# Optimization experiments

Measured on AMD Instinct MI355X. Metric: run time of the kernel, lower is better.

The kernel has to match this reference:

```python
import jax, jax.numpy as jnp
import numpy as np

EPS = 1e-5  # pyg LayerNorm default eps


def _graph_ln(x):
    # pyg.nn.norm.LayerNorm(affine=False), default mode='graph', batch=None:
    # normalizes over ALL elements of the tensor (x - x.mean()) / x.std(unbiased=False)
    m = x.mean()
    v = jnp.mean((x - m) ** 2)
    return (x - m) * jax.lax.rsqrt(v + EPS)


def _cheb_conv(x, row, col, w, W, b):
    # ChebConv, normalization='sym', lambda_max=2 => scaled Laplacian
    # L_hat = L - I = -D^{-1/2} A D^{-1/2} (self-loops removed, weighted)
    # x: [B,N,C_in], row/col: [E], w: [E], W: [K,C_in,C_out], b: [C_out]
    N = x.shape[1]
    w = jnp.where(row == col, 0.0, w)  # remove_self_loops
    deg = jnp.zeros((N,), x.dtype).at[row].add(w)
    dinv = jnp.where(deg > 0, jax.lax.rsqrt(jnp.maximum(deg, 1e-12)), 0.0)
    norm = -(dinv[row] * w * dinv[col])  # [E]

    def prop(t):  # out[i] += norm_e * t[j] for edge (j=row -> i=col)
        msg = norm[None, :, None] * t[:, row, :]  # [B,E,C]
        return jnp.zeros_like(t).at[:, col, :].add(msg)

    Tx0 = x
    out = jnp.einsum('bnc,cd->bnd', Tx0, W[0])
    Tx1 = prop(x)
    out = out + jnp.einsum('bnc,cd->bnd', Tx1, W[1])
    for k in range(2, W.shape[0]):
        Tx2 = 2.0 * prop(Tx1) - Tx0
        out = out + jnp.einsum('bnc,cd->bnd', Tx2, W[k])
        Tx0, Tx1 = Tx1, Tx2
    return out + b


def setup_inputs() -> dict:
    key = jax.random.key(0)
    ks = jax.random.split(key, 8)
    B, N, C, E, L, K = 8, 2048, 256, 32768, 3, 3
    node_feature = jax.random.normal(ks[0], (B, N, C), dtype=jnp.float32)
    edge_index = jax.random.randint(ks[1], (L, 2, E), 0, N)
    edge_weight = jax.random.uniform(ks[2], (L, E), dtype=jnp.float32)
    s = 1.0 / np.sqrt(C)
    cheb_w = jax.random.normal(ks[3], (L, K, C, C), dtype=jnp.float32) * s
    cheb_b = jnp.zeros((L, C), dtype=jnp.float32)
    mlp_w = jax.random.normal(ks[4], (L, C, C), dtype=jnp.float32) * s
    mlp_b = jax.random.normal(ks[5], (L, C), dtype=jnp.float32) * 0.01
    return {"node_feature": node_feature, "edge_weight": edge_weight,
            "cheb_w": cheb_w, "cheb_b": cheb_b, "mlp_w": mlp_w,
            "mlp_b": mlp_b, "edge_index": edge_index}


def reference(node_feature, edge_weight, cheb_w, cheb_b, mlp_w, mlp_b, edge_index):
    h = node_feature  # [B,N,C]
    L = cheb_w.shape[0]
    for l in range(L):
        h_res = h
        hn = _graph_ln(h)
        hc = _cheb_conv(hn, edge_index[l, 0], edge_index[l, 1],
                        edge_weight[l], cheb_w[l], cheb_b[l])
        h = hc + h_res
        h_res = h
        hn = _graph_ln(h)
        hm = jax.nn.gelu(jnp.einsum('bnc,cd->bnd', hn, mlp_w[l]) + mlp_b[l],
                         approximate=False)  # dropout is identity at inference
        h = hm + h_res
    return h.mean(axis=1)  # [B,C]
```

## Files before the change

### kernel.cpp

```cpp
#include <hip/hip_runtime.h>

#define BATCH   8
#define NNODE   2048
#define CH      256
#define NEDGE   32768
#define NLAYER  3
#define MROWS   (NNODE*BATCH)
#define KCAT    (3*CH)
#define NTOT    (MROWS*CH)

typedef _Float16 half8 __attribute__((ext_vector_type(8)));
typedef _Float16 half4 __attribute__((ext_vector_type(4)));
typedef float    f32x4 __attribute__((ext_vector_type(4)));

#define OFF_H      ((size_t)0)
#define OFF_ACAT   ((size_t)16777216)
#define OFF_HF     ((size_t)41943040)
#define OFF_WT     ((size_t)50331648)
#define OFF_MT     ((size_t)51511296)
#define OFF_PARTA  ((size_t)51904512)
#define OFF_PARTB  ((size_t)51912704)
#define OFF_CS     ((size_t)51920896)
#define OFF_CSM    ((size_t)51930112)
#define OFF_DEG    ((size_t)51933184)
#define OFF_CNT    ((size_t)51957760)
#define OFF_ELIST  ((size_t)51982336)
#define OFF_NORM   ((size_t)53555200)
#define OFF_R1     ((size_t)53948416)
#define OFF_R2     ((size_t)53972992)
#define OFF_MP     ((size_t)53997568)

__device__ __forceinline__ void async_lds16(const void* g, void* l) {
  __builtin_amdgcn_global_load_lds((const __attribute__((address_space(1))) void*)g,
                                   (__attribute__((address_space(3))) void*)l, 16, 0, 0);
}

__global__ __launch_bounds__(256) void k_init(const float* __restrict__ x,
                                              float* __restrict__ h,
                                              _Float16* __restrict__ Acat,
                                              float2* __restrict__ part,
                                              float* __restrict__ deg,
                                              unsigned int* __restrict__ count,
                                              float* __restrict__ r1) {
  const int blk = blockIdx.x;
  if (blk < 1024) {
    int tid = blk*256 + threadIdx.x;
    float s = 0.f, s2 = 0.f;
    for (int i = tid; i < NTOT/4; i += 1024*256) {
      int c4 = i & 63, b = (i >> 6) & 7, n = i >> 9;
      float4 v = ((const float4*)x)[((b*NNODE + n) << 6) + c4];
      ((float4*)h)[i] = v;
      half4 o; o[0]=(_Float16)v.x; o[1]=(_Float16)v.y; o[2]=(_Float16)v.z; o[3]=(_Float16)v.w;
      *(half4*)&Acat[(size_t)(i >> 6)*KCAT + c4*4] = o;
      s  += v.x + v.y + v.z + v.w;
      s2 += v.x*v.x + v.y*v.y + v.z*v.z + v.w*v.w;
    }
    __shared__ float rs[512];
    rs[threadIdx.x] = s; rs[256+threadIdx.x] = s2; __syncthreads();
    for (int o = 128; o > 0; o >>= 1) {
      if (threadIdx.x < o) { rs[threadIdx.x] += rs[threadIdx.x+o]; rs[256+threadIdx.x] += rs[256+threadIdx.x+o]; }
      __syncthreads();
    }
    if (threadIdx.x == 0) part[blk] = make_float2(rs[0], rs[256]);
  } else {
    int i = (blk - 1024)*256 + threadIdx.x;
    if (i < NLAYER*NNODE) { deg[i] = 0.f; count[i] = 0u; r1[i] = 0.f; }
  }
}

__global__ __launch_bounds__(256) void k_weights(const float* __restrict__ cheb_w,
                                                 const float* __restrict__ mlp_w,
                                                 _Float16* __restrict__ Wt,
                                                 _Float16* __restrict__ Mt) {
  __shared__ _Float16 lt[64][72];
  const int t = threadIdx.x;
  const int rr = t >> 4, c4 = t & 15;
  const int tile = blockIdx.x;
  if (tile < 144) {
    const int l = tile / 48, rem = tile % 48;
    const int kk = rem / 16, q = rem % 16, ci = q >> 2, ni = q & 3;
    const float4* W  = (const float4*)cheb_w + ((size_t)((l*3 + kk)*CH + ci*64))*64 + ni*16;
    const float4* W2 = (const float4*)cheb_w + ((size_t)((l*3 + 2 )*CH + ci*64))*64 + ni*16;
    #pragma unroll
    for (int p = 0; p < 4; ++p) {
      const int r = p*16 + rr;
      float4 v = W[(size_t)r*64 + c4];
      if (kk == 0) {
        float4 v2 = W2[(size_t)r*64 + c4];
        v.x -= v2.x; v.y -= v2.y; v.z -= v2.z; v.w -= v2.w;
      } else if (kk == 2) {
        v.x *= 2.f; v.y *= 2.f; v.z *= 2.f; v.w *= 2.f;
      }
      lt[c4*4+0][r] = (_Float16)v.x; lt[c4*4+1][r] = (_Float16)v.y;
      lt[c4*4+2][r] = (_Float16)v.z; lt[c4*4+3][r] = (_Float16)v.w;
    }
    __syncthreads();
    const int nr = t >> 2, ch2 = t & 3;
    #pragma unroll
    for (int pp = 0; pp < 2; ++pp) {
      const int ch = ch2 + pp*4;
      half8 v = *(const half8*)&lt[nr][ch*8];
      *(half8*)&Wt[((size_t)(l*CH + ni*64 + nr))*KCAT + kk*256 + ci*64 + ch*8] = v;
    }
  } else {
    const int m = tile - 144;
    const int l = m / 16, q = m % 16, ci = q >> 2, ni = q & 3;
    const float4* W = (const float4*)mlp_w + ((size_t)(l*CH + ci*64))*64 + ni*16;
    #pragma unroll
    for (int p = 0; p < 4; ++p) {
      const int r = p*16 + rr;
      float4 v = W[(size_t)r*64 + c4];
      lt[c4*4+0][r] = (_Float16)v.x; lt[c4*4+1][r] = (_Float16)v.y;
      lt[c4*4+2][r] = (_Float16)v.z; lt[c4*4+3][r] = (_Float16)v.w;
    }
    __syncthreads();
    const int nr = t >> 2, ch2 = t & 3;
    #pragma unroll
    for (int pp = 0; pp < 2; ++pp) {
      const int ch = ch2 + pp*4;
      half8 v = *(const half8*)&lt[nr][ch*8];
      *(half8*)&Mt[((size_t)(l*CH + ni*64 + nr))*CH + ci*64 + ch*8] = v;
    }
  }
}

__global__ __launch_bounds__(256) void k_edge_scatter(const int* __restrict__ ei,
                                                      const float* __restrict__ ew,
                                                      float* deg, unsigned int* count,
                                                      unsigned int* elist) {
  int i = blockIdx.x*256 + threadIdx.x;
  if (i >= NLAYER*NEDGE) return;
  int l = i / NEDGE, e = i % NEDGE;
  const int* rows = ei + l*2*NEDGE;
  const int* cols = rows + NEDGE;
  int r = rows[e], c = cols[e];
  float w = (r == c) ? 0.f : ew[l*NEDGE + e];
  atomicAdd(&deg[l*NNODE + r], w);
  unsigned int slot = atomicAdd(&count[l*NNODE + c], 1u);
  if (slot < 64u) elist[(l*NNODE + c)*64 + slot] = (unsigned int)e;
}

__global__ __launch_bounds__(256) void k_edge_norm(const int* __restrict__ ei,
                                                   const float* __restrict__ ew,
                                                   const float* __restrict__ deg,
                                                   float* __restrict__ norm,
                                                   float* __restrict__ r1) {
  int i = blockIdx.x*256 + threadIdx.x;
  if (i >= NLAYER*NEDGE) return;
  int l = i / NEDGE, e = i % NEDGE;
  const int* rows = ei + l*2*NEDGE;
  const int* cols = rows + NEDGE;
  int r = rows[e], c = cols[e];
  float w = (r == c) ? 0.f : ew[l*NEDGE + e];
  float dr = deg[l*NNODE + r], dc = deg[l*NNODE + c];
  float ir = dr > 0.f ? rsqrtf(fmaxf(dr, 1e-12f)) : 0.f;
  float ic = dc > 0.f ? rsqrtf(fmaxf(dc, 1e-12f)) : 0.f;
  float nm = -(ir * w * ic);
  norm[i] = nm;
  atomicAdd(&r1[l*NNODE + c], nm);
}

__global__ __launch_bounds__(256) void k_aux(const int* __restrict__ ei,
                                             const float* __restrict__ norm,
                                             const unsigned int* __restrict__ count,
                                             const unsigned int* __restrict__ elist,
                                             const float* __restrict__ r1,
                                             float* __restrict__ r2,
                                             const _Float16* __restrict__ Wt,
                                             const _Float16* __restrict__ Mt,
                                             float* __restrict__ cs,
                                             float* __restrict__ csM) {
  const int blk = blockIdx.x;
  if (blk < 24) {
    int i = blk*256 + threadIdx.x;
    int l = i / NNODE;
    const int* rows = ei + l*2*NEDGE;
    unsigned int c = count[i]; if (c > 64u) c = 64u;
    const unsigned int* el = elist + (size_t)i*64;
    float s = 0.f;
    for (unsigned int j = 0; j < c; ++j) {
      unsigned int e = el[j];
      s += norm[l*NEDGE + e] * r1[l*NNODE + rows[e]];
    }
    r2[i] = s;
  } else if (blk < 33) {
    int idx = blk - 24;
    int l = idx / 3, kk = idx % 3, n = threadIdx.x;
    const half8* row = (const half8*)&Wt[((size_t)(l*CH + n))*KCAT + kk*256];
    float s = 0.f;
    #pragma unroll 4
    for (int j = 0; j < 32; ++j) {
      half8 v = row[j];
      s += (float)v[0]+(float)v[1]+(float)v[2]+(float)v[3]
         + (float)v[4]+(float)v[5]+(float)v[6]+(float)v[7];
    }
    cs[(l*3 + kk)*CH + n] = s;
  } else {
    int l = blk - 33, n = threadIdx.x;
    const half8* row = (const half8*)&Mt[((size_t)(l*CH + n))*CH];
    float s = 0.f;
    #pragma unroll 4
    for (int j = 0; j < 32; ++j) {
      half8 v = row[j];
      s += (float)v[0]+(float)v[1]+(float)v[2]+(float)v[3]
         + (float)v[4]+(float)v[5]+(float)v[6]+(float)v[7];
    }
    csM[l*CH + n] = s;
  }
}

template<int SRC_OFF, int DST_OFF>
__global__ __launch_bounds__(64) void k_prop(_Float16* __restrict__ Acat,
                                             const int* __restrict__ rows,
                                             const float* __restrict__ norm,
                                             const unsigned int* __restrict__ count,
                                             const unsigned int* __restrict__ elist) {
  const int blk = blockIdx.x;
  const int b = blk & 7, dst = blk >> 3;
  const int lane = threadIdx.x;
  unsigned int cnt = count[dst]; if (cnt > 64u) cnt = 64u;
  int   srcv = 0;
  float nmv  = 0.f;
  if (lane < (int)cnt) {
    unsigned int e = elist[dst*64 + lane];
    srcv = rows[e];
    nmv  = norm[e];
  }
  float a0 = 0.f, a1 = 0.f, a2 = 0.f, a3 = 0.f;
  const _Float16* base = Acat + SRC_OFF + lane*4;
  #define PROP_STEP(i)                                                              \
    {                                                                               \
      int   src = __builtin_amdgcn_readlane(srcv, (i));                             \
      int   nbi = __builtin_amdgcn_readlane(__builtin_bit_cast(int, nmv), (i));     \
      float nm  = __builtin_bit_cast(float, nbi);                                   \
      half4 v = *(const half4*)&base[(size_t)(src*8 + b)*KCAT];                     \
      a0 += nm*(float)v[0]; a1 += nm*(float)v[1];                                   \
      a2 += nm*(float)v[2]; a3 += nm*(float)v[3];                                   \
    }
  unsigned int i = 0;
  for (; i + 4 <= cnt; i += 4) { PROP_STEP(i) PROP_STEP(i+1) PROP_STEP(i+2) PROP_STEP(i+3) }
  for (; i < cnt; ++i) { PROP_STEP(i) }
  #undef PROP_STEP
  half4 o; o[0] = (_Float16)a0; o[1] = (_Float16)a1; o[2] = (_Float16)a2; o[3] = (_Float16)a3;
  *(half4*)&Acat[(size_t)(dst*8 + b)*KCAT + DST_OFF + lane*4] = o;
}

template<int KSTEPS, int DO_GELU>
__global__ __launch_bounds__(256) void k_gemm(const _Float16* __restrict__ A, int lda,
                                              const _Float16* __restrict__ Bt, int ldb,
                                              const float* __restrict__ bias,
                                              const float* __restrict__ cs,
                                              const float* __restrict__ r1,
                                              const float* __restrict__ r2,
                                              const float2* __restrict__ part_in,
                                              float2* __restrict__ part_out,
                                              float* __restrict__ H,
                                              _Float16* __restrict__ Of, int ofs) {
  __shared__ _Float16 Als[64*64];
  __shared__ _Float16 Bls[64*64];
  __shared__ float red[512];
  __shared__ float mv[2];
  const int bm = blockIdx.x, bn = blockIdx.y;
  const int t = threadIdx.x;
  const int w = t >> 6, lane = t & 63;
  const int quad = lane >> 4, l16 = lane & 15;
  const int wm = w & 1, wn = w >> 1;

  {
    float s = 0.f, s2 = 0.f;
    for (int i = t; i < 1024; i += 256) { float2 p = part_in[i]; s += p.x; s2 += p.y; }
    red[t] = s; red[256+t] = s2; __syncthreads();
    for (int o = 128; o > 0; o >>= 1) {
      if (t < o) { red[t] += red[t+o]; red[256+t] += red[256+t+o]; }
      __syncthreads();
    }
    if (t == 0) {
      float mean = red[0] * (1.f/(float)NTOT);
      float var  = red[256] * (1.f/(float)NTOT) - mean*mean;
      mv[0] = mean; mv[1] = rsqrtf(var + 1e-5f);
    }
    __syncthreads();
  }
  const float mean = mv[0], istd = mv[1];

  f32x4 acc00 = {0.f,0.f,0.f,0.f};
  f32x4 acc01 = acc00, acc10 = acc00, acc11 = acc00;

  const int c0 = w*64 + lane, c1 = 256 + w*64 + lane;
  const int r0 = c0 >> 3, s0 = (c0 & 7) ^ (r0 & 7);
  const int r1i = c1 >> 3, s1 = (c1 & 7) ^ (r1i & 7);
  const _Float16* ga0 = A  + (size_t)(bm*64 + r0)*lda + s0*8;
  const _Float16* ga1 = A  + (size_t)(bm*64 + r1i)*lda + s1*8;
  const _Float16* gb0 = Bt + (size_t)(bn*64 + r0)*ldb + s0*8;
  const _Float16* gb1 = Bt + (size_t)(bn*64 + r1i)*ldb + s1*8;
  _Float16* lA0 = &Als[w*512];
  _Float16* lA1 = &Als[2048 + w*512];
  _Float16* lB0 = &Bls[w*512];
  _Float16* lB1 = &Bls[2048 + w*512];

  const int ra0 = wm*32 + l16, ra1 = ra0 + 16;
  const int rb0 = wn*32 + l16, rb1 = rb0 + 16;

  for (int ks = 0; ks < KSTEPS; ++ks) {
    async_lds16(ga0, lA0); async_lds16(ga1, lA1);
    async_lds16(gb0, lB0); async_lds16(gb1, lB1);
    ga0 += 64; ga1 += 64; gb0 += 64; gb1 += 64;
    __syncthreads();
    #pragma unroll
    for (int kh = 0; kh < 2; ++kh) {
      const int q = kh*4 + quad;
      half8 a0 = *(const half8*)&Als[ra0*64 + (q ^ (ra0 & 7))*8];
      half8 a1 = *(const half8*)&Als[ra1*64 + (q ^ (ra1 & 7))*8];
      half8 b0 = *(const half8*)&Bls[rb0*64 + (q ^ (rb0 & 7))*8];
      half8 b1 = *(const half8*)&Bls[rb1*64 + (q ^ (rb1 & 7))*8];
      acc00 = __builtin_amdgcn_mfma_f32_16x16x32_f16(a0, b0, acc00, 0, 0, 0);
      acc01 = __builtin_amdgcn_mfma_f32_16x16x32_f16(a0, b1, acc01, 0, 0, 0);
      acc10 = __builtin_amdgcn_mfma_f32_16x16x32_f16(a1, b0, acc10, 0, 0, 0);
      acc11 = __builtin_amdgcn_mfma_f32_16x16x32_f16(a1, b1, acc11, 0, 0, 0);
    }
    __syncthreads();
  }

  float s = 0.f, s2 = 0.f;
  const int gm0 = bm*64 + wm*32, gn0 = bn*64 + wn*32;
  const float mi = -mean * istd;
  #pragma unroll
  for (int i = 0; i < 2; ++i) {
    #pragma unroll
    for (int j = 0; j < 2; ++j) {
      f32x4 a = (i == 0) ? (j == 0 ? acc00 : acc01) : (j == 0 ? acc10 : acc11);
      const int col = gn0 + j*16 + l16;
      const float bv = bias[col];
      const float c0v = cs[col];
      float c1v = 0.f, c2v = 0.f;
      if (!DO_GELU) { c1v = cs[256 + col]; c2v = cs[512 + col]; }
      #pragma unroll
      for (int r = 0; r < 4; ++r) {
        const int row = gm0 + i*16 + quad*4 + r;
        float v;
        if (DO_GELU) {
          v = istd*a[r] + mi*c0v + bv;
          v = 0.5f*v*(1.f + erff(v*0.70710678118654752f));
        } else {
          const int node = row >> 3;
          v = istd*a[r] + mi*(c0v + r1[node]*c1v + r2[node]*c2v) + bv;
        }
        float hv = H[(size_t)row*CH + col] + v;
        H[(size_t)row*CH + col] = hv;
        Of[(size_t)row*ofs + col] = (_Float16)hv;
        s += hv; s2 += hv*hv;
      }
    }
  }
  red[t] = s; red[256+t] = s2; __syncthreads();
  for (int o = 128; o > 0; o >>= 1) {
    if (t < o) { red[t] += red[t+o]; red[256+t] += red[256+t+o]; }
    __syncthreads();
  }
  if (t == 0) part_out[blockIdx.y*gridDim.x + blockIdx.x] = make_float2(red[0], red[256]);
}

__global__ __launch_bounds__(256) void k_mean_part(const float* __restrict__ h,
                                                   float* __restrict__ mp) {
  int blk = blockIdx.x;
  int b = blk & 7, chunk = blk >> 3;
  int c = threadIdx.x;
  float s = 0.f;
  for (int k = 0; k < 32; ++k) {
    int n = chunk*32 + k;
    s += h[((size_t)(n*8 + b) << 8) + c];
  }
  mp[((b*64 + chunk) << 8) + c] = s;
}

__global__ __launch_bounds__(256) void k_mean_final(const float* __restrict__ mp,
                                                    float* __restrict__ out) {
  int b = blockIdx.x, c = threadIdx.x;
  float s = 0.f;
  for (int ch = 0; ch < 64; ++ch) s += mp[((b*64 + ch) << 8) + c];
  out[(b << 8) + c] = s * (1.f/(float)NNODE);
}

extern "C" void kernel_launch(void* const* d_in, const int* in_sizes, int n_in,
                              void* d_out, int out_size, void* d_ws, size_t ws_size,
                              hipStream_t stream) {
  const float* x      = (const float*)d_in[0];
  const float* ew     = (const float*)d_in[1];
  const float* cheb_w = (const float*)d_in[2];
  const float* cheb_b = (const float*)d_in[3];
  const float* mlp_w  = (const float*)d_in[4];
  const float* mlp_b  = (const float*)d_in[5];
  const int*   ei     = (const int*)d_in[6];
  float* out = (float*)d_out;

  char* ws = (char*)d_ws;
  float*        h     = (float*)(ws + OFF_H);
  _Float16*     Acat  = (_Float16*)(ws + OFF_ACAT);
  _Float16*     Hf    = (_Float16*)(ws + OFF_HF);
  _Float16*     Wt    = (_Float16*)(ws + OFF_WT);
  _Float16*     Mt    = (_Float16*)(ws + OFF_MT);
  float2*       partA = (float2*)(ws + OFF_PARTA);
  float2*       partB = (float2*)(ws + OFF_PARTB);
  float*        cs    = (float*)(ws + OFF_CS);
  float*        csM   = (float*)(ws + OFF_CSM);
  float*        deg   = (float*)(ws + OFF_DEG);
  unsigned int* cnt   = (unsigned int*)(ws + OFF_CNT);
  unsigned int* elist = (unsigned int*)(ws + OFF_ELIST);
  float*        norm  = (float*)(ws + OFF_NORM);
  float*        r1    = (float*)(ws + OFF_R1);
  float*        r2    = (float*)(ws + OFF_R2);
  float*        mp    = (float*)(ws + OFF_MP);

  k_init<<<1048, 256, 0, stream>>>(x, h, Acat, partA, deg, cnt, r1);
  k_weights<<<192, 256, 0, stream>>>(cheb_w, mlp_w, Wt, Mt);
  k_edge_scatter<<<(NLAYER*NEDGE)/256, 256, 0, stream>>>(ei, ew, deg, cnt, elist);
  k_edge_norm<<<(NLAYER*NEDGE)/256, 256, 0, stream>>>(ei, ew, deg, norm, r1);
  k_aux<<<36, 256, 0, stream>>>(ei, norm, cnt, elist, r1, r2, Wt, Mt, cs, csM);

  for (int l = 0; l < NLAYER; ++l) {
    const int* rows_l = ei + l*2*NEDGE;
    const unsigned int* cnt_l = cnt + l*NNODE;
    const unsigned int* el_l  = elist + (size_t)l*NNODE*64;
    const float* norm_l = norm + l*NEDGE;

    k_prop<0, 256><<<MROWS, 64, 0, stream>>>(Acat, rows_l, norm_l, cnt_l, el_l);
    k_prop<256, 512><<<MROWS, 64, 0, stream>>>(Acat, rows_l, norm_l, cnt_l, el_l);
    k_gemm<12, 0><<<dim3(256, 4), 256, 0, stream>>>(
        Acat, KCAT, Wt + (size_t)l*CH*KCAT, KCAT, cheb_b + l*CH,
        cs + l*3*CH, r1 + l*NNODE, r2 + l*NNODE, partA, partB, h, Hf, CH);
    k_gemm<4, 1><<<dim3(256, 4), 256, 0, stream>>>(
        Hf, CH, Mt + (size_t)l*CH*CH, CH, mlp_b + l*CH,
        csM + l*CH, r1, r2, partB, partA, h, Acat, KCAT);
  }

  k_mean_part<<<512, 256, 0, stream>>>(h, mp);
  k_mean_final<<<8, 256, 0, stream>>>(mp, out);
}
```

Baseline: 317.3 us.

## Fuse all stages into one persistent cooperative kernel with grid syncs

```diff
diff --git a/kernel.cpp b/kernel.cpp
--- a/kernel.cpp
+++ b/kernel.cpp
@@ -1,4 +1,7 @@
 #include <hip/hip_runtime.h>
+#include <hip/hip_cooperative_groups.h>
+
+namespace cg = cooperative_groups;
 
 #define BATCH   8
 #define NNODE   2048
@@ -30,52 +33,21 @@
 #define OFF_R2     ((size_t)53972992)
 #define OFF_MP     ((size_t)53997568)
 
+#define SMEM_BYTES 18448
+
 __device__ __forceinline__ void async_lds16(const void* g, void* l) {
   __builtin_amdgcn_global_load_lds((const __attribute__((address_space(1))) void*)g,
                                    (__attribute__((address_space(3))) void*)l, 16, 0, 0);
 }
 
-__global__ __launch_bounds__(256) void k_init(const float* __restrict__ x,
-                                              float* __restrict__ h,
-                                              _Float16* __restrict__ Acat,
-                                              float2* __restrict__ part,
-                                              float* __restrict__ deg,
-                                              unsigned int* __restrict__ count,
-                                              float* __restrict__ r1) {
-  const int blk = blockIdx.x;
-  if (blk < 1024) {
-    int tid = blk*256 + threadIdx.x;
-    float s = 0.f, s2 = 0.f;
-    for (int i = tid; i < NTOT/4; i += 1024*256) {
-      int c4 = i & 63, b = (i >> 6) & 7, n = i >> 9;
-      float4 v = ((const float4*)x)[((b*NNODE + n) << 6) + c4];
-      ((float4*)h)[i] = v;
-      half4 o; o[0]=(_Float16)v.x; o[1]=(_Float16)v.y; o[2]=(_Float16)v.z; o[3]=(_Float16)v.w;
-      *(half4*)&Acat[(size_t)(i >> 6)*KCAT + c4*4] = o;
-      s  += v.x + v.y + v.z + v.w;
-      s2 += v.x*v.x + v.y*v.y + v.z*v.z + v.w*v.w;
-    }
-    __shared__ float rs[512];
-    rs[threadIdx.x] = s; rs[256+threadIdx.x] = s2; __syncthreads();
-    for (int o = 128; o > 0; o >>= 1) {
-      if (threadIdx.x < o) { rs[threadIdx.x] += rs[threadIdx.x+o]; rs[256+threadIdx.x] += rs[256+threadIdx.x+o]; }
-      __syncthreads();
-    }
-    if (threadIdx.x == 0) part[blk] = make_float2(rs[0], rs[256]);
-  } else {
-    int i = (blk - 1024)*256 + threadIdx.x;
-    if (i < NLAYER*NNODE) { deg[i] = 0.f; count[i] = 0u; r1[i] = 0.f; }
-  }
-}
-
-__global__ __launch_bounds__(256) void k_weights(const float* __restrict__ cheb_w,
-                                                 const float* __restrict__ mlp_w,
-                                                 _Float16* __restrict__ Wt,
-                                                 _Float16* __restrict__ Mt) {
-  __shared__ _Float16 lt[64][72];
-  const int t = threadIdx.x;
+__device__ __forceinline__ void weights_tile(int tile, int t,
+                                             const float* __restrict__ cheb_w,
+                                             const float* __restrict__ mlp_w,
+                                             _Float16* __restrict__ Wt,
+                                             _Float16* __restrict__ Mt,
+                                             char* smem) {
+  _Float16 (*lt)[72] = (_Float16(*)[72])smem;
   const int rr = t >> 4, c4 = t & 15;
-  const int tile = blockIdx.x;
   if (tile < 144) {
     const int l = tile / 48, rem = tile % 48;
     const int kk = rem / 16, q = rem % 16, ci = q >> 2, ni = q & 3;
@@ -124,143 +96,62 @@
   }
 }
 
-__global__ __launch_bounds__(256) void k_edge_scatter(const int* __restrict__ ei,
-                                                      const float* __restrict__ ew,
-                                                      float* deg, unsigned int* count,
-                                                      unsigned int* elist) {
-  int i = blockIdx.x*256 + threadIdx.x;
-  if (i >= NLAYER*NEDGE) return;
-  int l = i / NEDGE, e = i % NEDGE;
-  const int* rows = ei + l*2*NEDGE;
-  const int* cols = rows + NEDGE;
-  int r = rows[e], c = cols[e];
-  float w = (r == c) ? 0.f : ew[l*NEDGE + e];
-  atomicAdd(&deg[l*NNODE + r], w);
-  unsigned int slot = atomicAdd(&count[l*NNODE + c], 1u);
-  if (slot < 64u) elist[(l*NNODE + c)*64 + slot] = (unsigned int)e;
-}
-
-__global__ __launch_bounds__(256) void k_edge_norm(const int* __restrict__ ei,
-                                                   const float* __restrict__ ew,
-                                                   const float* __restrict__ deg,
-                                                   float* __restrict__ norm,
-                                                   float* __restrict__ r1) {
-  int i = blockIdx.x*256 + threadIdx.x;
-  if (i >= NLAYER*NEDGE) return;
-  int l = i / NEDGE, e = i % NEDGE;
-  const int* rows = ei + l*2*NEDGE;
-  const int* cols = rows + NEDGE;
-  int r = rows[e], c = cols[e];
-  float w = (r == c) ? 0.f : ew[l*NEDGE + e];
-  float dr = deg[l*NNODE + r], dc = deg[l*NNODE + c];
-  float ir = dr > 0.f ? rsqrtf(fmaxf(dr, 1e-12f)) : 0.f;
-  float ic = dc > 0.f ? rsqrtf(fmaxf(dc, 1e-12f)) : 0.f;
-  float nm = -(ir * w * ic);
-  norm[i] = nm;
-  atomicAdd(&r1[l*NNODE + c], nm);
-}
-
-__global__ __launch_bounds__(256) void k_aux(const int* __restrict__ ei,
-                                             const float* __restrict__ norm,
-                                             const unsigned int* __restrict__ count,
-                                             const unsigned int* __restrict__ elist,
-                                             const float* __restrict__ r1,
-                                             float* __restrict__ r2,
-                                             const _Float16* __restrict__ Wt,
-                                             const _Float16* __restrict__ Mt,
-                                             float* __restrict__ cs,
-                                             float* __restrict__ csM) {
-  const int blk = blockIdx.x;
-  if (blk < 24) {
-    int i = blk*256 + threadIdx.x;
-    int l = i / NNODE;
-    const int* rows = ei + l*2*NEDGE;
-    unsigned int c = count[i]; if (c > 64u) c = 64u;
-    const unsigned int* el = elist + (size_t)i*64;
-    float s = 0.f;
-    for (unsigned int j = 0; j < c; ++j) {
-      unsigned int e = el[j];
-      s += norm[l*NEDGE + e] * r1[l*NNODE + rows[e]];
-    }
-    r2[i] = s;
-  } else if (blk < 33) {
-    int idx = blk - 24;
-    int l = idx / 3, kk = idx % 3, n = threadIdx.x;
-    const half8* row = (const half8*)&Wt[((size_t)(l*CH + n))*KCAT + kk*256];
-    float s = 0.f;
-    #pragma unroll 4
-    for (int j = 0; j < 32; ++j) {
-      half8 v = row[j];
-      s += (float)v[0]+(float)v[1]+(float)v[2]+(float)v[3]
-         + (float)v[4]+(float)v[5]+(float)v[6]+(float)v[7];
-    }
-    cs[(l*3 + kk)*CH + n] = s;
-  } else {
-    int l = blk - 33, n = threadIdx.x;
-    const half8* row = (const half8*)&Mt[((size_t)(l*CH + n))*CH];
-    float s = 0.f;
-    #pragma unroll 4
-    for (int j = 0; j < 32; ++j) {
-      half8 v = row[j];
-      s += (float)v[0]+(float)v[1]+(float)v[2]+(float)v[3]
-         + (float)v[4]+(float)v[5]+(float)v[6]+(float)v[7];
-    }
-    csM[l*CH + n] = s;
-  }
-}
-
-template<int SRC_OFF, int DST_OFF>
-__global__ __launch_bounds__(64) void k_prop(_Float16* __restrict__ Acat,
-                                             const int* __restrict__ rows,
-                                             const float* __restrict__ norm,
-                                             const unsigned int* __restrict__ count,
-                                             const unsigned int* __restrict__ elist) {
-  const int blk = blockIdx.x;
-  const int b = blk & 7, dst = blk >> 3;
-  const int lane = threadIdx.x;
-  unsigned int cnt = count[dst]; if (cnt > 64u) cnt = 64u;
-  int   srcv = 0;
-  float nmv  = 0.f;
-  if (lane < (int)cnt) {
-    unsigned int e = elist[dst*64 + lane];
-    srcv = rows[e];
-    nmv  = norm[e];
-  }
-  float a0 = 0.f, a1 = 0.f, a2 = 0.f, a3 = 0.f;
-  const _Float16* base = Acat + SRC_OFF + lane*4;
-  #define PROP_STEP(i)                                                              \
-    {                                                                               \
-      int   src = __builtin_amdgcn_readlane(srcv, (i));                             \
-      int   nbi = __builtin_amdgcn_readlane(__builtin_bit_cast(int, nmv), (i));     \
-      float nm  = __builtin_bit_cast(float, nbi);                                   \
-      half4 v = *(const half4*)&base[(size_t)(src*8 + b)*KCAT];                     \
-      a0 += nm*(float)v[0]; a1 += nm*(float)v[1];                                   \
-      a2 += nm*(float)v[2]; a3 += nm*(float)v[3];                                   \
-    }
-  unsigned int i = 0;
-  for (; i + 4 <= cnt; i += 4) { PROP_STEP(i) PROP_STEP(i+1) PROP_STEP(i+2) PROP_STEP(i+3) }
-  for (; i < cnt; ++i) { PROP_STEP(i) }
-  #undef PROP_STEP
-  half4 o; o[0] = (_Float16)a0; o[1] = (_Float16)a1; o[2] = (_Float16)a2; o[3] = (_Float16)a3;
-  *(half4*)&Acat[(size_t)(dst*8 + b)*KCAT + DST_OFF + lane*4] = o;
+__device__ __forceinline__ void prop_phase(_Float16* __restrict__ Acat,
+                                           int src_off, int dst_off,
+                                           const int* __restrict__ rows,
+                                           const float* __restrict__ nrm,
+                                           const unsigned int* __restrict__ count,
+                                           const unsigned int* __restrict__ el) {
+  const int w = threadIdx.x >> 6, lane = threadIdx.x & 63;
+  const int stride = gridDim.x*4;
+  for (int g = blockIdx.x*4 + w; g < 4096; g += stride) {
+    const int dst = g >> 1, bb = (g & 1) << 2;
+    unsigned int c = count[dst]; if (c > 64u) c = 64u;
+    int srcv = 0; float nmv = 0.f;
+    if (lane < (int)c) {
+      unsigned int e = el[(size_t)dst*64 + lane];
+      srcv = rows[e]; nmv = nrm[e];
+    }
+    float acc[4][4] = {{0.f,0.f,0.f,0.f},{0.f,0.f,0.f,0.f},{0.f,0.f,0.f,0.f},{0.f,0.f,0.f,0.f}};
+    const _Float16* base = Acat + src_off + lane*4;
+    for (unsigned int i = 0; i < c; ++i) {
+      int   src = __builtin_amdgcn_readlane(srcv, i);
+      int   nbi = __builtin_amdgcn_readlane(__builtin_bit_cast(int, nmv), i);
+      float nm  = __builtin_bit_cast(float, nbi);
+      const _Float16* p = base + (size_t)(src*8 + bb)*KCAT;
+      #pragma unroll
+      for (int j = 0; j < 4; ++j) {
+        half4 v = *(const half4*)(p + (size_t)j*KCAT);
+        acc[j][0] += nm*(float)v[0]; acc[j][1] += nm*(float)v[1];
+        acc[j][2] += nm*(float)v[2]; acc[j][3] += nm*(float)v[3];
+      }
+    }
+    #pragma unroll
+    for (int j = 0; j < 4; ++j) {
+      half4 o; o[0]=(_Float16)acc[j][0]; o[1]=(_Float16)acc[j][1];
+      o[2]=(_Float16)acc[j][2]; o[3]=(_Float16)acc[j][3];
+      *(half4*)&Acat[(size_t)(dst*8 + bb + j)*KCAT + dst_off + lane*4] = o;
+    }
+  }
 }
 
 template<int KSTEPS, int DO_GELU>
-__global__ __launch_bounds__(256) void k_gemm(const _Float16* __restrict__ A, int lda,
-                                              const _Float16* __restrict__ Bt, int ldb,
-                                              const float* __restrict__ bias,
-                                              const float* __restrict__ cs,
-                                              const float* __restrict__ r1,
-                                              const float* __restrict__ r2,
-                                              const float2* __restrict__ part_in,
-                                              float2* __restrict__ part_out,
-                                              float* __restrict__ H,
-                                              _Float16* __restrict__ Of, int ofs) {
-  __shared__ _Float16 Als[64*64];
-  __shared__ _Float16 Bls[64*64];
-  __shared__ float red[512];
-  __shared__ float mv[2];
-  const int bm = blockIdx.x, bn = blockIdx.y;
+__device__ __forceinline__ void gemm_phase(const _Float16* __restrict__ A, int lda,
+                                           const _Float16* __restrict__ Bt, int ldb,
+                                           const float* __restrict__ bias,
+                                           const float* __restrict__ csv,
+                                           const float* __restrict__ r1v,
+                                           const float* __restrict__ r2v,
+                                           const float2* __restrict__ part_in,
+                                           float2* __restrict__ part_out,
+                                           float* __restrict__ H,
+                                           _Float16* __restrict__ Of, int ofs,
+                                           char* smem) {
+  _Float16* Als = (_Float16*)smem;
+  _Float16* Bls = (_Float16*)(smem + 8192);
+  float* red = (float*)(smem + 16384);
+  float* mv  = (float*)(smem + 18432);
+  const int NB = gridDim.x;
   const int t = threadIdx.x;
   const int w = t >> 6, lane = t & 63;
   const int quad = lane >> 4, l16 = lane & 15;
@@ -268,7 +159,7 @@
 
   {
     float s = 0.f, s2 = 0.f;
-    for (int i = t; i < 1024; i += 256) { float2 p = part_in[i]; s += p.x; s2 += p.y; }
+    for (int i = t; i < NB; i += 256) { float2 p = part_in[i]; s += p.x; s2 += p.y; }
     red[t] = s; red[256+t] = s2; __syncthreads();
     for (int o = 128; o > 0; o >>= 1) {
       if (t < o) { red[t] += red[t+o]; red[256+t] += red[256+t+o]; }
@@ -282,103 +173,235 @@
     __syncthreads();
   }
   const float mean = mv[0], istd = mv[1];
-
-  f32x4 acc00 = {0.f,0.f,0.f,0.f};
-  f32x4 acc01 = acc00, acc10 = acc00, acc11 = acc00;
+  const float mi = -mean * istd;
 
   const int c0 = w*64 + lane, c1 = 256 + w*64 + lane;
   const int r0 = c0 >> 3, s0 = (c0 & 7) ^ (r0 & 7);
   const int r1i = c1 >> 3, s1 = (c1 & 7) ^ (r1i & 7);
-  const _Float16* ga0 = A  + (size_t)(bm*64 + r0)*lda + s0*8;
-  const _Float16* ga1 = A  + (size_t)(bm*64 + r1i)*lda + s1*8;
-  const _Float16* gb0 = Bt + (size_t)(bn*64 + r0)*ldb + s0*8;
-  const _Float16* gb1 = Bt + (size_t)(bn*64 + r1i)*ldb + s1*8;
   _Float16* lA0 = &Als[w*512];
   _Float16* lA1 = &Als[2048 + w*512];
   _Float16* lB0 = &Bls[w*512];
   _Float16* lB1 = &Bls[2048 + w*512];
-
   const int ra0 = wm*32 + l16, ra1 = ra0 + 16;
   const int rb0 = wn*32 + l16, rb1 = rb0 + 16;
 
-  for (int ks = 0; ks < KSTEPS; ++ks) {
-    async_lds16(ga0, lA0); async_lds16(ga1, lA1);
-    async_lds16(gb0, lB0); async_lds16(gb1, lB1);
-    ga0 += 64; ga1 += 64; gb0 += 64; gb1 += 64;
+  float s = 0.f, s2 = 0.f;
+  for (int vt = blockIdx.x; vt < 1024; vt += NB) {
+    const int bm = vt & 255, bn = vt >> 8;
+    f32x4 acc00 = {0.f,0.f,0.f,0.f};
+    f32x4 acc01 = acc00, acc10 = acc00, acc11 = acc00;
+    const _Float16* ga0 = A  + (size_t)(bm*64 + r0)*lda + s0*8;
+    const _Float16* ga1 = A  + (size_t)(bm*64 + r1i)*lda + s1*8;
+    const _Float16* gb0 = Bt + (size_t)(bn*64 + r0)*ldb + s0*8;
+    const _Float16* gb1 = Bt + (size_t)(bn*64 + r1i)*ldb + s1*8;
     __syncthreads();
-    #pragma unroll
-    for (int kh = 0; kh < 2; ++kh) {
-      const int q = kh*4 + quad;
-      half8 a0 = *(const half8*)&Als[ra0*64 + (q ^ (ra0 & 7))*8];
-      half8 a1 = *(const half8*)&Als[ra1*64 + (q ^ (ra1 & 7))*8];
-      half8 b0 = *(const half8*)&Bls[rb0*64 + (q ^ (rb0 & 7))*8];
-      half8 b1 = *(const half8*)&Bls[rb1*64 + (q ^ (rb1 & 7))*8];
-      acc00 = __builtin_amdgcn_mfma_f32_16x16x32_f16(a0, b0, acc00, 0, 0, 0);
-      acc01 = __builtin_amdgcn_mfma_f32_16x16x32_f16(a0, b1, acc01, 0, 0, 0);
-      acc10 = __builtin_amdgcn_mfma_f32_16x16x32_f16(a1, b0, acc10, 0, 0, 0);
-      acc11 = __builtin_amdgcn_mfma_f32_16x16x32_f16(a1, b1, acc11, 0, 0, 0);
-    }
-    __syncthreads();
-  }
-
-  float s = 0.f, s2 = 0.f;
-  const int gm0 = bm*64 + wm*32, gn0 = bn*64 + wn*32;
-  const float mi = -mean * istd;
-  #pragma unroll
-  for (int i = 0; i < 2; ++i) {
-    #pragma unroll
-    for (int j = 0; j < 2; ++j) {
-      f32x4 a = (i == 0) ? (j == 0 ? acc00 : acc01) : (j == 0 ? acc10 : acc11);
-      const int col = gn0 + j*16 + l16;
-      const float bv = bias[col];
-      const float c0v = cs[col];
-      float c1v = 0.f, c2v = 0.f;
-      if (!DO_GELU) { c1v = cs[256 + col]; c2v = cs[512 + col]; }
+    for (int ks = 0; ks < KSTEPS; ++ks) {
+      async_lds16(ga0, lA0); async_lds16(ga1, lA1);
+      async_lds16(gb0, lB0); async_lds16(gb1, lB1);
+      ga0 += 64; ga1 += 64; gb0 += 64; gb1 += 64;
+      __syncthreads();
       #pragma unroll
-      for (int r = 0; r < 4; ++r) {
-        const int row = gm0 + i*16 + quad*4 + r;
-        float v;
-        if (DO_GELU) {
-          v = istd*a[r] + mi*c0v + bv;
-          v = 0.5f*v*(1.f + erff(v*0.70710678118654752f));
-        } else {
-          const int node = row >> 3;
-          v = istd*a[r] + mi*(c0v + r1[node]*c1v + r2[node]*c2v) + bv;
+      for (int kh = 0; kh < 2; ++kh) {
+        const int q = kh*4 + quad;
+        half8 a0 = *(const half8*)&Als[ra0*64 + (q ^ (ra0 & 7))*8];
+        half8 a1 = *(const half8*)&Als[ra1*64 + (q ^ (ra1 & 7))*8];
+        half8 b0 = *(const half8*)&Bls[rb0*64 + (q ^ (rb0 & 7))*8];
+        half8 b1 = *(const half8*)&Bls[rb1*64 + (q ^ (rb1 & 7))*8];
+        acc00 = __builtin_amdgcn_mfma_f32_16x16x32_f16(a0, b0, acc00, 0, 0, 0);
+        acc01 = __builtin_amdgcn_mfma_f32_16x16x32_f16(a0, b1, acc01, 0, 0, 0);
+        acc10 = __builtin_amdgcn_mfma_f32_16x16x32_f16(a1, b0, acc10, 0, 0, 0);
+        acc11 = __builtin_amdgcn_mfma_f32_16x16x32_f16(a1, b1, acc11, 0, 0, 0);
+      }
+      __syncthreads();
+    }
+
+    const int gm0 = bm*64 + wm*32, gn0 = bn*64 + wn*32;
+    #pragma unroll
+    for (int i = 0; i < 2; ++i) {
+      #pragma unroll
+      for (int j = 0; j < 2; ++j) {
+        f32x4 a = (i == 0) ? (j == 0 ? acc00 : acc01) : (j == 0 ? acc10 : acc11);
+        const int col = gn0 + j*16 + l16;
+        const float bv = bias[col];
+        const float c0v = csv[col];
+        float c1v = 0.f, c2v = 0.f;
+        if (!DO_GELU) { c1v = csv[256 + col]; c2v = csv[512 + col]; }
+        #pragma unroll
+        for (int r = 0; r < 4; ++r) {
+          const int row = gm0 + i*16 + quad*4 + r;
+          float v;
+          if (DO_GELU) {
+            v = istd*a[r] + mi*c0v + bv;
+            v = 0.5f*v*(1.f + erff(v*0.70710678118654752f));
+          } else {
+            const int node = row >> 3;
+            v = istd*a[r] + mi*(c0v + r1v[node]*c1v + r2v[node]*c2v) + bv;
+          }
+          float hv = H[(size_t)row*CH + col] + v;
+          H[(size_t)row*CH + col] = hv;
+          Of[(size_t)row*ofs + col] = (_Float16)hv;
+          s += hv; s2 += hv*hv;
         }
-        float hv = H[(size_t)row*CH + col] + v;
-        H[(size_t)row*CH + col] = hv;
-        Of[(size_t)row*ofs + col] = (_Float16)hv;
-        s += hv; s2 += hv*hv;
-      }
-    }
-  }
+      }
+    }
+  }
+  __syncthreads();
   red[t] = s; red[256+t] = s2; __syncthreads();
   for (int o = 128; o > 0; o >>= 1) {
     if (t < o) { red[t] += red[t+o]; red[256+t] += red[256+t+o]; }
     __syncthreads();
   }
-  if (t == 0) part_out[blockIdx.y*gridDim.x + blockIdx.x] = make_float2(red[0], red[256]);
-}
-
-__global__ __launch_bounds__(256) void k_mean_part(const float* __restrict__ h,
-                                                   float* __restrict__ mp) {
-  int blk = blockIdx.x;
-  int b = blk & 7, chunk = blk >> 3;
-  int c = threadIdx.x;
-  float s = 0.f;
-  for (int k = 0; k < 32; ++k) {
-    int n = chunk*32 + k;
-    s += h[((size_t)(n*8 + b) << 8) + c];
-  }
-  mp[((b*64 + chunk) << 8) + c] = s;
-}
-
-__global__ __launch_bounds__(256) void k_mean_final(const float* __restrict__ mp,
-                                                    float* __restrict__ out) {
-  int b = blockIdx.x, c = threadIdx.x;
-  float s = 0.f;
-  for (int ch = 0; ch < 64; ++ch) s += mp[((b*64 + ch) << 8) + c];
-  out[(b << 8) + c] = s * (1.f/(float)NNODE);
+  if (t == 0) part_out[blockIdx.x] = make_float2(red[0], red[256]);
+  __syncthreads();
+}
+
+extern "C" __global__ __launch_bounds__(256, 2)
+void k_mega(const float* __restrict__ x, const float* __restrict__ ew,
+            const float* __restrict__ cheb_w, const float* __restrict__ cheb_b,
+            const float* __restrict__ mlp_w, const float* __restrict__ mlp_b,
+            const int* __restrict__ ei, float* __restrict__ out,
+            float* __restrict__ h, _Float16* __restrict__ Acat,
+            _Float16* __restrict__ Hf, _Float16* __restrict__ Wt,
+            _Float16* __restrict__ Mt, float2* __restrict__ partA,
+            float2* __restrict__ partB, float* __restrict__ cs,
+            float* __restrict__ csM, float* __restrict__ deg,
+            unsigned int* __restrict__ cntp, unsigned int* __restrict__ elist,
+            float* __restrict__ norm, float* __restrict__ r1,
+            float* __restrict__ r2, float* __restrict__ mp) {
+  cg::grid_group grid = cg::this_grid();
+  __shared__ __align__(16) char smem[SMEM_BYTES];
+  const int blk = blockIdx.x, t = threadIdx.x;
+  const int NB = gridDim.x;
+  const int tid = blk*256 + t;
+  const int nthreads = NB*256;
+
+  {
+    float* rs = (float*)smem;
+    float s = 0.f, s2 = 0.f;
+    for (int i = tid; i < NTOT/4; i += nthreads) {
+      int c4 = i & 63, b = (i >> 6) & 7, n = i >> 9;
+      float4 v = ((const float4*)x)[((b*NNODE + n) << 6) + c4];
+      ((float4*)h)[i] = v;
+      half4 o; o[0]=(_Float16)v.x; o[1]=(_Float16)v.y; o[2]=(_Float16)v.z; o[3]=(_Float16)v.w;
+      *(half4*)&Acat[(size_t)(i >> 6)*KCAT + c4*4] = o;
+      s  += v.x + v.y + v.z + v.w;
+      s2 += v.x*v.x + v.y*v.y + v.z*v.z + v.w*v.w;
+    }
+    rs[t] = s; rs[256+t] = s2; __syncthreads();
+    for (int o = 128; o > 0; o >>= 1) {
+      if (t < o) { rs[t] += rs[t+o]; rs[256+t] += rs[256+t+o]; }
+      __syncthreads();
+    }
+    if (t == 0) partA[blk] = make_float2(rs[0], rs[256]);
+    for (int i = tid; i < NLAYER*NNODE; i += nthreads) { deg[i] = 0.f; cntp[i] = 0u; r1[i] = 0.f; }
+    for (int tile = blk; tile < 192; tile += NB) {
+      __syncthreads();
+      weights_tile(tile, t, cheb_w, mlp_w, Wt, Mt, smem);
+    }
+  }
+  grid.sync();
+
+  for (int i = tid; i < NLAYER*NEDGE; i += nthreads) {
+    int l = i / NEDGE, e = i % NEDGE;
+    const int* rows = ei + l*2*NEDGE;
+    const int* cols = rows + NEDGE;
+    int r = rows[e], c = cols[e];
+    float wv = (r == c) ? 0.f : ew[i];
+    atomicAdd(&deg[l*NNODE + r], wv);
+    unsigned int slot = atomicAdd(&cntp[l*NNODE + c], 1u);
+    if (slot < 64u) elist[(size_t)(l*NNODE + c)*64 + slot] = (unsigned int)e;
+  }
+  grid.sync();
+
+  for (int i = tid; i < NLAYER*NEDGE; i += nthreads) {
+    int l = i / NEDGE, e = i % NEDGE;
+    const int* rows = ei + l*2*NEDGE;
+    const int* cols = rows + NEDGE;
+    int r = rows[e], c = cols[e];
+    float wv = (r == c) ? 0.f : ew[i];
+    float dr = deg[l*NNODE + r], dc = deg[l*NNODE + c];
+    float ir = dr > 0.f ? rsqrtf(fmaxf(dr, 1e-12f)) : 0.f;
+    float ic = dc > 0.f ? rsqrtf(fmaxf(dc, 1e-12f)) : 0.f;
+    float nm = -(ir * wv * ic);
+    norm[i] = nm;
+    atomicAdd(&r1[l*NNODE + c], nm);
+  }
+  grid.sync();
+
+  for (int i = tid; i < 9216; i += nthreads) {
+    if (i < NLAYER*NNODE) {
+      int l = i / NNODE;
+      const int* rows = ei + l*2*NEDGE;
+      unsigned int c = cntp[i]; if (c > 64u) c = 64u;
+      const unsigned int* el = elist + (size_t)i*64;
+      float s = 0.f;
+      for (unsigned int j = 0; j < c; ++j) {
+        unsigned int e = el[j];
+        s += norm[l*NEDGE + e] * r1[l*NNODE + rows[e]];
+      }
+      r2[i] = s;
+    } else if (i < 8448) {
+      int j = i - 6144, idx = j >> 8, n = j & 255;
+      int l = idx / 3, kk = idx % 3;
+      const half8* row = (const half8*)&Wt[((size_t)(l*CH + n))*KCAT + kk*256];
+      float s = 0.f;
+      #pragma unroll 4
+      for (int k = 0; k < 32; ++k) {
+        half8 v = row[k];
+        s += (float)v[0]+(float)v[1]+(float)v[2]+(float)v[3]
+           + (float)v[4]+(float)v[5]+(float)v[6]+(float)v[7];
+      }
+      cs[idx*CH + n] = s;
+    } else {
+      int j = i - 8448, l = j >> 8, n = j & 255;
+      const half8* row = (const half8*)&Mt[((size_t)(l*CH + n))*CH];
+      float s = 0.f;
+      #pragma unroll 4
+      for (int k = 0; k < 32; ++k) {
+        half8 v = row[k];
+        s += (float)v[0]+(float)v[1]+(float)v[2]+(float)v[3]
+           + (float)v[4]+(float)v[5]+(float)v[6]+(float)v[7];
+      }
+      csM[l*CH + n] = s;
+    }
+  }
+  grid.sync();
+
+  for (int l = 0; l < NLAYER; ++l) {
+    const int* rows_l = ei + l*2*NEDGE;
+    const unsigned int* cnt_l = cntp + l*NNODE;
+    const unsigned int* el_l  = elist + (size_t)l*NNODE*64;
+    const float* norm_l = norm + l*NEDGE;
+
+    prop_phase(Acat, 0, 256, rows_l, norm_l, cnt_l, el_l);
+    grid.sync();
+    prop_phase(Acat, 256, 512, rows_l, norm_l, cnt_l, el_l);
+    grid.sync();
+    gemm_phase<12, 0>(Acat, KCAT, Wt + (size_t)l*CH*KCAT, KCAT,
+                      cheb_b + l*CH, cs + l*3*CH, r1 + l*NNODE, r2 + l*NNODE,
+                      partA, partB, h, Hf, CH, smem);
+    grid.sync();
+    gemm_phase<4, 1>(Hf, CH, Mt + (size_t)l*CH*CH, CH,
+                     mlp_b + l*CH, csM + l*CH, r1, r2,
+                     partB, partA, h, Acat, KCAT, smem);
+    grid.sync();
+  }
+
+  for (int v = blk; v < 512; v += NB) {
+    int b = v & 7, chunk = v >> 3;
+    float s = 0.f;
+    for (int k = 0; k < 32; ++k) {
+      int n = chunk*32 + k;
+      s += h[((size_t)(n*8 + b) << 8) + t];
+    }
+    mp[((b*64 + chunk) << 8) + t] = s;
+  }
+  grid.sync();
+  if (blk < 8) {
+    float s = 0.f;
+    for (int ch = 0; ch < 64; ++ch) s += mp[((blk*64 + ch) << 8) + t];
+    out[(blk << 8) + t] = s * (1.f/(float)NNODE);
+  }
 }
 
 extern "C" void kernel_launch(void* const* d_in, const int* in_sizes, int n_in,
@@ -404,35 +427,21 @@
   float*        cs    = (float*)(ws + OFF_CS);
   float*        csM   = (float*)(ws + OFF_CSM);
   float*        deg   = (float*)(ws + OFF_DEG);
-  unsigned int* cnt   = (unsigned int*)(ws + OFF_CNT);
+  unsigned int* cntp  = (unsigned int*)(ws + OFF_CNT);
   unsigned int* elist = (unsigned int*)(ws + OFF_ELIST);
   float*        norm  = (float*)(ws + OFF_NORM);
   float*        r1    = (float*)(ws + OFF_R1);
   float*        r2    = (float*)(ws + OFF_R2);
   float*        mp    = (float*)(ws + OFF_MP);
 
-  k_init<<<1048, 256, 0, stream>>>(x, h, Acat, partA, deg, cnt, r1);
-  k_weights<<<192, 256, 0, stream>>>(cheb_w, mlp_w, Wt, Mt);
-  k_edge_scatter<<<(NLAYER*NEDGE)/256, 256, 0, stream>>>(ei, ew, deg, cnt, elist);
-  k_edge_norm<<<(NLAYER*NEDGE)/256, 256, 0, stream>>>(ei, ew, deg, norm, r1);
-  k_aux<<<36, 256, 0, stream>>>(ei, norm, cnt, elist, r1, r2, Wt, Mt, cs, csM);
-
-  for (int l = 0; l < NLAYER; ++l) {
-    const int* rows_l = ei + l*2*NEDGE;
-    const unsigned int* cnt_l = cnt + l*NNODE;
-    const unsigned int* el_l  = elist + (size_t)l*NNODE*64;
-    const float* norm_l = norm + l*NEDGE;
-
-    k_prop<0, 256><<<MROWS, 64, 0, stream>>>(Acat, rows_l, norm_l, cnt_l, el_l);
-    k_prop<256, 512><<<MROWS, 64, 0, stream>>>(Acat, rows_l, norm_l, cnt_l, el_l);
-    k_gemm<12, 0><<<dim3(256, 4), 256, 0, stream>>>(
-        Acat, KCAT, Wt + (size_t)l*CH*KCAT, KCAT, cheb_b + l*CH,
-        cs + l*3*CH, r1 + l*NNODE, r2 + l*NNODE, partA, partB, h, Hf, CH);
-    k_gemm<4, 1><<<dim3(256, 4), 256, 0, stream>>>(
-        Hf, CH, Mt + (size_t)l*CH*CH, CH, mlp_b + l*CH,
-        csM + l*CH, r1, r2, partB, partA, h, Acat, KCAT);
-  }
-
-  k_mean_part<<<512, 256, 0, stream>>>(h, mp);
-  k_mean_final<<<8, 256, 0, stream>>>(mp, out);
-}
+  int nb = 0;
+  if (hipOccupancyMaxActiveBlocksPerMultiprocessor(&nb, (const void*)k_mega, 256, 0)
+        != hipSuccess || nb < 1) nb = 2;
+  int grid = nb * 256;
+  if (grid > 1024) grid = 1024;
+
+  void* args[] = { &x, &ew, &cheb_w, &cheb_b, &mlp_w, &mlp_b, &ei, &out,
+                   &h, &Acat, &Hf, &Wt, &Mt, &partA, &partB, &cs, &csM,
+                   &deg, &cntp, &elist, &norm, &r1, &r2, &mp };
+  hipLaunchCooperativeKernel((void*)k_mega, dim3(grid), dim3(256), args, 0, stream);
+}
```

After: 1.022 ms. 3.22x slower.
